# Kernel tuning notes

Hardware: AMD Instinct MI355X
Metric: run time of the kernel (lower is better)

## Reference

```python
import jax, jax.numpy as jnp
import numpy as np


def sage_conv(x, src, dst, n, W_l, b_l, W_r):
    # PyG SAGEConv (mean aggr): out = lin_l(mean_{j in N(i)} x_j) + lin_r(x_i)
    msg = x[src]                                            # [E, d_in] gather
    s = jax.ops.segment_sum(msg, dst, num_segments=n)       # [N, d_in]
    cnt = jax.ops.segment_sum(jnp.ones((src.shape[0], 1), x.dtype), dst, num_segments=n)
    mean = s / jnp.maximum(cnt, 1.0)
    return mean @ W_l.T + b_l + x @ W_r.T


def setup_inputs() -> dict:
    key = jax.random.key(0)
    ks = jax.random.split(key, 12)
    N, E, D = 200000, 6400000, 128
    x = jax.random.normal(ks[0], (N, D), dtype=jnp.float32)
    edge_index = jax.random.randint(ks[1], (2, E), 0, N, dtype=jnp.int64)

    def lin(k, dout, din, scale=None):
        s = scale if scale is not None else 1.0 / np.sqrt(din)
        return jax.random.uniform(k, (dout, din), jnp.float32, -s, s)

    return {
        "x": x,
        "edge_index": edge_index,
        "W1_l": lin(ks[2], 64, D), "b1_l": jnp.zeros((64,), jnp.float32), "W1_r": lin(ks[3], 64, D),
        "W2_l": lin(ks[4], 32, 64), "b2_l": jnp.zeros((32,), jnp.float32), "W2_r": lin(ks[5], 32, 64),
        "W3_l": lin(ks[6], 16, 32), "b3_l": jnp.zeros((16,), jnp.float32), "W3_r": lin(ks[7], 16, 32),
        "W_reg": lin(ks[8], 1, 16), "b_reg": jnp.zeros((1,), jnp.float32),
        "W_cls": lin(ks[9], 1, 16), "b_cls": jnp.zeros((1,), jnp.float32),
    }


def reference(x, edge_index, W1_l, b1_l, W1_r, W2_l, b2_l, W2_r, W3_l, b3_l, W3_r,
              W_reg, b_reg, W_cls, b_cls):
    # eval mode: dropout is identity
    n = x.shape[0]
    src, dst = edge_index[0], edge_index[1]
    h = jax.nn.relu(sage_conv(x, src, dst, n, W1_l, b1_l, W1_r))
    h = jax.nn.relu(sage_conv(h, src, dst, n, W2_l, b2_l, W2_r))
    h = jax.nn.relu(sage_conv(h, src, dst, n, W3_l, b3_l, W3_r))
    reg = (h @ W_reg.T + b_reg)[:, 0]
    cls = (h @ W_cls.T + b_cls)[:, 0]
    return (reg, cls)
```

## Files before the change

kernel.cpp:

```cpp
#include <hip/hip_runtime.h>


typedef __bf16 bf16x8 __attribute__((ext_vector_type(8)));
typedef float  f32x4  __attribute__((ext_vector_type(4)));
typedef int    i32x4  __attribute__((ext_vector_type(4)));

__device__ __forceinline__ unsigned short f2bf_rne(float f) {
    unsigned int u = __float_as_uint(f);
    u = (u + 0x7FFFu + ((u >> 16) & 1u)) >> 16;
    return (unsigned short)u;
}

__device__ __forceinline__ void bfacc(float4& a, const uint2 q) {
    a.x += __uint_as_float(q.x << 16);
    a.y += __uint_as_float(q.x & 0xFFFF0000u);
    a.z += __uint_as_float(q.y << 16);
    a.w += __uint_as_float(q.y & 0xFFFF0000u);
}


__global__ __launch_bounds__(256) void k_bcount(const int* __restrict__ dst, int E, int N,
                                                int* __restrict__ bcnt) {
    __shared__ int h[256];
    const int tid = threadIdx.x;
    h[tid] = 0;
    __syncthreads();
    const int stride = gridDim.x * 256;
    for (int i = blockIdx.x * 256 + tid; i < E; i += stride) {
        int d = dst[i];
        d = d < 0 ? 0 : (d >= N ? N - 1 : d);
        atomicAdd(&h[d >> 10], 1);
    }
    __syncthreads();
    if (h[tid]) atomicAdd(&bcnt[tid], h[tid]);
}

__global__ __launch_bounds__(256) void k_bscan(const int* __restrict__ bcnt,
                                               int* __restrict__ boff,
                                               int* __restrict__ bcur, int NBK, int E) {
    __shared__ int sd[256];
    const int tid = threadIdx.x;
    bcur[tid] = 0;
    int v = (tid < NBK) ? bcnt[tid] : 0;
    sd[tid] = v; __syncthreads();
    for (int off = 1; off < 256; off <<= 1) {
        int t = (tid >= off) ? sd[tid - off] : 0;
        __syncthreads();
        sd[tid] += t;
        __syncthreads();
    }
    if (tid < NBK) boff[tid] = sd[tid] - v;
    if (tid == 0) boff[NBK] = E;
}

#define BTILE 4096
__global__ __launch_bounds__(256) void k_bucket(const int* __restrict__ src,
                                                const int* __restrict__ dst, int E, int N,
                                                const int* __restrict__ boff,
                                                int* __restrict__ bcur,
                                                int* __restrict__ T, int NBK) {
    __shared__ int cnt[256], cnt2[256], lofs[256], gbase[256], boffs[256], sd[256];
    __shared__ int2 staged[BTILE];
    const int tid = threadIdx.x;
    const int tb = blockIdx.x * BTILE;
    const int tn = min(BTILE, E - tb);
    cnt[tid] = 0; cnt2[tid] = 0;
    boffs[tid] = (tid < NBK) ? boff[tid] : 0;
    __syncthreads();
    for (int i = tid; i < tn; i += 256) {
        int d = dst[tb + i];
        d = d < 0 ? 0 : (d >= N ? N - 1 : d);
        atomicAdd(&cnt[d >> 10], 1);
    }
    __syncthreads();
    int v = cnt[tid];
    sd[tid] = v; __syncthreads();
    for (int off = 1; off < 256; off <<= 1) {
        int t = (tid >= off) ? sd[tid - off] : 0;
        __syncthreads();
        sd[tid] += t;
        __syncthreads();
    }
    lofs[tid] = sd[tid] - v;
    if (v > 0 && tid < NBK) gbase[tid] = atomicAdd(&bcur[tid], v);
    __syncthreads();
    for (int i = tid; i < tn; i += 256) {
        int d = dst[tb + i];
        d = d < 0 ? 0 : (d >= N ? N - 1 : d);
        int s = src[tb + i];
        s = s < 0 ? 0 : (s >= N ? N - 1 : s);
        int b = d >> 10;
        int r = atomicAdd(&cnt2[b], 1);
        staged[lofs[b] + r] = make_int2(s, d);
    }
    __syncthreads();
    for (int i = tid; i < tn; i += 256) {
        int2 p = staged[i];
        int b = p.y >> 10;
        T[(size_t)boffs[b] + gbase[b] + (i - lofs[b])] = ((p.y & 1023) << 18) | p.x;
    }
}

__global__ __launch_bounds__(1024) void k_csr(const int* __restrict__ T,
                                              const int* __restrict__ boff,
                                              int* __restrict__ rowptr,
                                              int* __restrict__ adj, int N, int E) {
    __shared__ int hist[1024];
    __shared__ int sc[1024];
    const int tid = threadIdx.x;
    const int b = blockIdx.x;
    const int node0 = b << 10;
    hist[tid] = 0;
    __syncthreads();
    const int beg = boff[b], end = boff[b + 1];
    for (int i = beg + tid; i < end; i += 1024)
        atomicAdd(&hist[((unsigned)T[i]) >> 18], 1);
    __syncthreads();
    int v = hist[tid];
    sc[tid] = v;
    __syncthreads();
    for (int off = 1; off < 1024; off <<= 1) {
        int t = (tid >= off) ? sc[tid - off] : 0;
        __syncthreads();
        sc[tid] += t;
        __syncthreads();
    }
    const int excl = beg + sc[tid] - v;
    const int n = node0 + tid;
    if (n < N) rowptr[n] = excl;
    if (b == 0 && tid == 0) rowptr[N] = E;
    hist[tid] = excl;
    __syncthreads();
    for (int i = beg + tid; i < end; i += 1024) {
        unsigned p = (unsigned)T[i];
        int pos = atomicAdd(&hist[p >> 18], 1);
        adj[pos] = (int)(p & 0x3FFFFu);
    }
}

template<int DIN, int DOUT>
__global__ __launch_bounds__(256) void proj_mfma(const float* __restrict__ H,
                                                 const float* __restrict__ Wl,
                                                 const float* __restrict__ Wr,
                                                 const float* __restrict__ bias,
                                                 unsigned short* __restrict__ Pl,
                                                 float* __restrict__ R, int N) {
    constexpr int SP = DIN + 8;
    constexpr int COLT = DOUT / 16;
    __shared__ __bf16 lwl[DOUT * SP];
    __shared__ __bf16 lwrh[DOUT * SP];
    __shared__ __bf16 lwrl[DOUT * SP];
    for (int idx = threadIdx.x; idx < DIN * DOUT; idx += 256) {
        int c = idx / DIN, k = idx % DIN;
        float wl = Wl[idx], wr = Wr[idx];
        __bf16 wrh = (__bf16)wr;
        lwl[c * SP + k] = (__bf16)wl;
        lwrh[c * SP + k] = wrh;
        lwrl[c * SP + k] = (__bf16)(wr - (float)wrh);
    }
    __syncthreads();
    const int wave = threadIdx.x >> 6, lane = threadIdx.x & 63;
    const int quad = lane >> 4, l16 = lane & 15;
    const int n0 = (blockIdx.x * 4 + wave) * 16;
    int arow = n0 + l16;
    if (arow >= N) arow = N - 1;
    const float* hrow = H + (size_t)arow * DIN;

    f32x4 zero = {0.f, 0.f, 0.f, 0.f};
    f32x4 accP[COLT], accR[COLT];
    #pragma unroll
    for (int t = 0; t < COLT; ++t) { accP[t] = zero; accR[t] = zero; }

    for (int k0 = 0; k0 < DIN; k0 += 32) {
        const float* hp = hrow + k0 + quad * 8;
        float4 h0 = *(const float4*)hp;
        float4 h1 = *(const float4*)(hp + 4);
        float hv[8] = {h0.x, h0.y, h0.z, h0.w, h1.x, h1.y, h1.z, h1.w};
        bf16x8 ahi, alo;
        #pragma unroll
        for (int j = 0; j < 8; ++j) {
            __bf16 hb = (__bf16)hv[j];
            ahi[j] = hb;
            alo[j] = (__bf16)(hv[j] - (float)hb);
        }
        const int kk = k0 + quad * 8;
        #pragma unroll
        for (int t = 0; t < COLT; ++t) {
            const int c = t * 16 + l16;
            bf16x8 bl  = *(const bf16x8*)&lwl [c * SP + kk];
            bf16x8 brh = *(const bf16x8*)&lwrh[c * SP + kk];
            bf16x8 brl = *(const bf16x8*)&lwrl[c * SP + kk];
            accP[t] = __builtin_amdgcn_mfma_f32_16x16x32_bf16(ahi, bl,  accP[t], 0, 0, 0);
            accR[t] = __builtin_amdgcn_mfma_f32_16x16x32_bf16(ahi, brh, accR[t], 0, 0, 0);
            accR[t] = __builtin_amdgcn_mfma_f32_16x16x32_bf16(ahi, brl, accR[t], 0, 0, 0);
            accR[t] = __builtin_amdgcn_mfma_f32_16x16x32_bf16(alo, brh, accR[t], 0, 0, 0);
        }
    }
    #pragma unroll
    for (int t = 0; t < COLT; ++t) {
        const int c = t * 16 + l16;
        const float bc = bias[c];
        #pragma unroll
        for (int r = 0; r < 4; ++r) {
            int node = n0 + quad * 4 + r;
            if (node < N) {
                Pl[(size_t)node * DOUT + c] = f2bf_rne(accP[t][r]);
                R[(size_t)node * DOUT + c] = accR[t][r] + bc;
            }
        }
    }
}


template<int DOUT> struct GatherCfg {
    static constexpr int L   = DOUT / 4;
    static constexpr int S   = 64 / L;
    static constexpr int M   = 4;
    static constexpr int NPW = S * M;
    static constexpr int NPB = NPW * 4;
};

template<int DOUT, bool HEAD>
__global__ __launch_bounds__(256, 6) void gather_kernel(const unsigned short* __restrict__ P,
                                                        const int* __restrict__ rowptr,
                                                        const int* __restrict__ adj,
                                                        float* __restrict__ Hout, int N,
                                                        const float* __restrict__ Wreg,
                                                        const float* __restrict__ breg,
                                                        const float* __restrict__ Wcls,
                                                        const float* __restrict__ bcls,
                                                        float* __restrict__ out) {
    using C = GatherCfg<DOUT>;
    constexpr int L = C::L, S = C::S, M = C::M;
    constexpr int NPW = C::NPW, NPB = C::NPB;
    const int wave = threadIdx.x >> 6, lane = threadIdx.x & 63;
    const int sub = lane / L, cl = lane % L;
    const uint2* __restrict__ P2 = (const uint2*)P;
    f32x4* __restrict__ H4 = (f32x4*)Hout;
    const int base = blockIdx.x * NPB + wave * NPW + sub;
    #pragma unroll 1
    for (int m = 0; m < M; ++m) {
        int n = base + m * S;
        if (n >= N) continue;
        int beg = __builtin_nontemporal_load(rowptr + n);
        int end = __builtin_nontemporal_load(rowptr + n + 1);
        float4 a0 = {0, 0, 0, 0}, a1 = {0, 0, 0, 0}, a2 = {0, 0, 0, 0}, a3 = {0, 0, 0, 0};
        int j = beg;
        while (j < end && (j & 3)) { bfacc(a0, P2[(size_t)adj[j] * L + cl]); ++j; }
        for (; j + 8 <= end; j += 8) {
            i32x4 sA = __builtin_nontemporal_load((const i32x4*)(adj + j));
            i32x4 sB = __builtin_nontemporal_load((const i32x4*)(adj + j + 4));
            uint2 p0 = P2[(size_t)sA.x * L + cl];
            uint2 p1 = P2[(size_t)sA.y * L + cl];
            uint2 p2 = P2[(size_t)sA.z * L + cl];
            uint2 p3 = P2[(size_t)sA.w * L + cl];
            uint2 p4 = P2[(size_t)sB.x * L + cl];
            uint2 p5 = P2[(size_t)sB.y * L + cl];
            uint2 p6 = P2[(size_t)sB.z * L + cl];
            uint2 p7 = P2[(size_t)sB.w * L + cl];
            bfacc(a0, p0); bfacc(a1, p1); bfacc(a2, p2); bfacc(a3, p3);
            bfacc(a0, p4); bfacc(a1, p5); bfacc(a2, p6); bfacc(a3, p7);
        }
        if (j + 4 <= end) {
            i32x4 sA = __builtin_nontemporal_load((const i32x4*)(adj + j));
            bfacc(a0, P2[(size_t)sA.x * L + cl]);
            bfacc(a1, P2[(size_t)sA.y * L + cl]);
            bfacc(a2, P2[(size_t)sA.z * L + cl]);
            bfacc(a3, P2[(size_t)sA.w * L + cl]);
            j += 4;
        }
        for (; j < end; ++j) bfacc(a0, P2[(size_t)adj[j] * L + cl]);
        int deg = end - beg;
        float inv = deg > 0 ? 1.0f / (float)deg : 0.0f;
        f32x4 r = __builtin_nontemporal_load(&H4[(size_t)n * L + cl]);
        f32x4 o;
        o.x = fmaxf((a0.x + a1.x + a2.x + a3.x) * inv + r.x, 0.0f);
        o.y = fmaxf((a0.y + a1.y + a2.y + a3.y) * inv + r.y, 0.0f);
        o.z = fmaxf((a0.z + a1.z + a2.z + a3.z) * inv + r.z, 0.0f);
        o.w = fmaxf((a0.w + a1.w + a2.w + a3.w) * inv + r.w, 0.0f);
        if constexpr (HEAD) {
            float4 wr = ((const float4*)Wreg)[cl];
            float4 wc = ((const float4*)Wcls)[cl];
            float pr = o.x * wr.x + o.y * wr.y + o.z * wr.z + o.w * wr.w;
            float pc = o.x * wc.x + o.y * wc.y + o.z * wc.z + o.w * wc.w;
            pr += __shfl_xor(pr, 1); pr += __shfl_xor(pr, 2);
            pc += __shfl_xor(pc, 1); pc += __shfl_xor(pc, 2);
            if (cl == 0) {
                out[n] = pr + breg[0];
                out[(size_t)N + n] = pc + bcls[0];
            }
        } else {
            __builtin_nontemporal_store(o, &H4[(size_t)n * L + cl]);
        }
    }
}

extern "C" void kernel_launch(void* const* d_in, const int* in_sizes, int n_in,
                              void* d_out, int out_size, void* d_ws, size_t ws_size,
                              hipStream_t stream) {
    const float* x    = (const float*)d_in[0];
    const int*   ei   = (const int*)d_in[1];
    const float* W1l  = (const float*)d_in[2];
    const float* b1l  = (const float*)d_in[3];
    const float* W1r  = (const float*)d_in[4];
    const float* W2l  = (const float*)d_in[5];
    const float* b2l  = (const float*)d_in[6];
    const float* W2r  = (const float*)d_in[7];
    const float* W3l  = (const float*)d_in[8];
    const float* b3l  = (const float*)d_in[9];
    const float* W3r  = (const float*)d_in[10];
    const float* Wreg = (const float*)d_in[11];
    const float* breg = (const float*)d_in[12];
    const float* Wcls = (const float*)d_in[13];
    const float* bcls = (const float*)d_in[14];

    const int N = in_sizes[0] / 128;
    const int E = in_sizes[1] / 2;
    const int* src = ei;
    const int* dst = ei + E;

    char* ws = (char*)d_ws;
    size_t off = 0;
    auto alloc = [&](size_t bytes) -> void* {
        void* p = ws + off;
        off += (bytes + 255) & ~(size_t)255;
        return p;
    };
    int*   rowptr = (int*)alloc((size_t)(N + 1) * 4);
    int*   bcnt   = (int*)alloc(1024);
    int*   bcur   = (int*)alloc(1024);
    int*   boff   = (int*)alloc(1028);
    int*   adj    = (int*)alloc((size_t)E * 4);
    unsigned short* A = (unsigned short*)alloc((size_t)N * 64 * 2);
    float* B      = (float*)alloc((size_t)N * 64 * 4);
    float* C      = (float*)alloc((size_t)N * 32 * 4);
    float* D      = (float*)alloc((size_t)N * 16 * 4);
    int*   T      = (int*)B;

    const int NBK = (N + 1023) >> 10;

    hipMemsetAsync(bcnt, 0, 1024, stream);
    k_bcount<<<1024, 256, 0, stream>>>(dst, E, N, bcnt);
    k_bscan<<<1, 256, 0, stream>>>(bcnt, boff, bcur, NBK, E);
    k_bucket<<<(E + BTILE - 1) / BTILE, 256, 0, stream>>>(src, dst, E, N, boff, bcur, T, NBK);
    k_csr<<<NBK, 1024, 0, stream>>>(T, boff, rowptr, adj, N, E);

    const int PB = 64;
    constexpr int G64 = GatherCfg<64>::NPB;
    constexpr int G32 = GatherCfg<32>::NPB;
    constexpr int G16 = GatherCfg<16>::NPB;

    proj_mfma<128, 64><<<(N + PB - 1) / PB, 256, 0, stream>>>(x, W1l, W1r, b1l, A, B, N);
    gather_kernel<64, false><<<(N + G64 - 1) / G64, 256, 0, stream>>>(
        A, rowptr, adj, B, N, nullptr, nullptr, nullptr, nullptr, nullptr);
    proj_mfma<64, 32><<<(N + PB - 1) / PB, 256, 0, stream>>>(B, W2l, W2r, b2l, A, C, N);
    gather_kernel<32, false><<<(N + G32 - 1) / G32, 256, 0, stream>>>(
        A, rowptr, adj, C, N, nullptr, nullptr, nullptr, nullptr, nullptr);
    proj_mfma<32, 16><<<(N + PB - 1) / PB, 256, 0, stream>>>(C, W3l, W3r, b3l, A, D, N);
    gather_kernel<16, true><<<(N + G16 - 1) / G16, 256, 0, stream>>>(
        A, rowptr, adj, D, N, Wreg, breg, Wcls, bcls, (float*)d_out);
}
```

Measured before the change: 772.3 us.

## Fuse neighbor gather with next layer's projection via LDS staging

Merges each layer's mean-aggregation gather with the following layer's MFMA projection. The post-ReLU hidden rows are staged in shared memory and multiplied by the next weights, so the fp32 hidden activations are no longer written to and re-read from global memory. This also removes two kernel launches. It double-buffers the bf16 projection outputs (A1/A2) so a fused kernel never reads and writes the same buffer. It also drops the nontemporal load/store hints. In exchange there is more register and LDS pressure in the gather kernel, a block-wide barrier, and weights are reloaded and converted per block.

```diff
diff --git a/kernel.cpp b/kernel.cpp
--- a/kernel.cpp
+++ b/kernel.cpp
@@ -3,7 +3,6 @@
 
 typedef __bf16 bf16x8 __attribute__((ext_vector_type(8)));
 typedef float  f32x4  __attribute__((ext_vector_type(4)));
-typedef int    i32x4  __attribute__((ext_vector_type(4)));
 
 __device__ __forceinline__ unsigned short f2bf_rne(float f) {
     unsigned int u = __float_as_uint(f);
@@ -211,6 +210,137 @@
     }
 }
 
+template<int D, int DP>
+__global__ __launch_bounds__(256, 6) void gather_proj(const unsigned short* __restrict__ P,
+                                                      const int* __restrict__ rowptr,
+                                                      const int* __restrict__ adj,
+                                                      const float* __restrict__ Rres,
+                                                      const float* __restrict__ Wl,
+                                                      const float* __restrict__ Wr,
+                                                      const float* __restrict__ bias,
+                                                      unsigned short* __restrict__ Pout,
+                                                      float* __restrict__ Rout, int N) {
+    constexpr int L   = D / 4;
+    constexpr int S   = 64 / L;
+    constexpr int M   = 4;
+    constexpr int NPW = S * M;
+    constexpr int NPB = NPW * 4;
+    constexpr int SP  = D + 4;
+    constexpr int COLT = DP / 16;
+    __shared__ __align__(16) float hstage[NPB * SP];
+
+    const int wave = threadIdx.x >> 6, lane = threadIdx.x & 63;
+    const int sub = lane / L, cl = lane % L;
+    const uint2* __restrict__ P2 = (const uint2*)P;
+    const f32x4* __restrict__ R4 = (const f32x4*)Rres;
+    const int base = blockIdx.x * NPB + wave * NPW + sub;
+
+    #pragma unroll 1
+    for (int m = 0; m < M; ++m) {
+        const int n = base + m * S;
+        const int lrow = wave * NPW + sub + m * S;
+        f32x4 o = {0.f, 0.f, 0.f, 0.f};
+        if (n < N) {
+            int beg = rowptr[n], end = rowptr[n + 1];
+            float4 a0 = {0, 0, 0, 0}, a1 = {0, 0, 0, 0}, a2 = {0, 0, 0, 0}, a3 = {0, 0, 0, 0};
+            int j = beg;
+            while (j < end && (j & 3)) { bfacc(a0, P2[(size_t)adj[j] * L + cl]); ++j; }
+            for (; j + 8 <= end; j += 8) {
+                int4 sA = *(const int4*)(adj + j);
+                int4 sB = *(const int4*)(adj + j + 4);
+                uint2 p0 = P2[(size_t)sA.x * L + cl];
+                uint2 p1 = P2[(size_t)sA.y * L + cl];
+                uint2 p2 = P2[(size_t)sA.z * L + cl];
+                uint2 p3 = P2[(size_t)sA.w * L + cl];
+                uint2 p4 = P2[(size_t)sB.x * L + cl];
+                uint2 p5 = P2[(size_t)sB.y * L + cl];
+                uint2 p6 = P2[(size_t)sB.z * L + cl];
+                uint2 p7 = P2[(size_t)sB.w * L + cl];
+                bfacc(a0, p0); bfacc(a1, p1); bfacc(a2, p2); bfacc(a3, p3);
+                bfacc(a0, p4); bfacc(a1, p5); bfacc(a2, p6); bfacc(a3, p7);
+            }
+            if (j + 4 <= end) {
+                int4 sA = *(const int4*)(adj + j);
+                bfacc(a0, P2[(size_t)sA.x * L + cl]);
+                bfacc(a1, P2[(size_t)sA.y * L + cl]);
+                bfacc(a2, P2[(size_t)sA.z * L + cl]);
+                bfacc(a3, P2[(size_t)sA.w * L + cl]);
+                j += 4;
+            }
+            for (; j < end; ++j) bfacc(a0, P2[(size_t)adj[j] * L + cl]);
+            int deg = end - beg;
+            float inv = deg > 0 ? 1.0f / (float)deg : 0.0f;
+            f32x4 r = R4[(size_t)n * L + cl];
+            o.x = fmaxf((a0.x + a1.x + a2.x + a3.x) * inv + r.x, 0.0f);
+            o.y = fmaxf((a0.y + a1.y + a2.y + a3.y) * inv + r.y, 0.0f);
+            o.z = fmaxf((a0.z + a1.z + a2.z + a3.z) * inv + r.z, 0.0f);
+            o.w = fmaxf((a0.w + a1.w + a2.w + a3.w) * inv + r.w, 0.0f);
+        }
+        *(f32x4*)&hstage[lrow * SP + cl * 4] = o;
+    }
+    __syncthreads();
+
+    const int quad = lane >> 4, l16 = lane & 15;
+    f32x4 zero = {0.f, 0.f, 0.f, 0.f};
+    #pragma unroll
+    for (int tile = 0; tile < NPB / 64; ++tile) {
+        const int trow0 = wave * NPW + tile * 16;
+        f32x4 accP[COLT], accR[COLT];
+        #pragma unroll
+        for (int t = 0; t < COLT; ++t) { accP[t] = zero; accR[t] = zero; }
+        #pragma unroll
+        for (int k0 = 0; k0 < D; k0 += 32) {
+            const int kk = k0 + quad * 8;
+            const float* hp = &hstage[(trow0 + l16) * SP + kk];
+            bf16x8 ahi, alo;
+            #pragma unroll
+            for (int j = 0; j < 8; ++j) {
+                float hv = hp[j];
+                __bf16 hb = (__bf16)hv;
+                ahi[j] = hb;
+                alo[j] = (__bf16)(hv - (float)hb);
+            }
+            #pragma unroll
+            for (int t = 0; t < COLT; ++t) {
+                const int c = t * 16 + l16;
+                const float* wlp = Wl + c * D + kk;
+                const float* wrp = Wr + c * D + kk;
+                float4 wl0 = *(const float4*)wlp;
+                float4 wl1 = *(const float4*)(wlp + 4);
+                float4 wr0 = *(const float4*)wrp;
+                float4 wr1 = *(const float4*)(wrp + 4);
+                float wlv[8] = {wl0.x, wl0.y, wl0.z, wl0.w, wl1.x, wl1.y, wl1.z, wl1.w};
+                float wrv[8] = {wr0.x, wr0.y, wr0.z, wr0.w, wr1.x, wr1.y, wr1.z, wr1.w};
+                bf16x8 bl, brh, brl;
+                #pragma unroll
+                for (int j = 0; j < 8; ++j) {
+                    bl[j] = (__bf16)wlv[j];
+                    __bf16 wh = (__bf16)wrv[j];
+                    brh[j] = wh;
+                    brl[j] = (__bf16)(wrv[j] - (float)wh);
+                }
+                accP[t] = __builtin_amdgcn_mfma_f32_16x16x32_bf16(ahi, bl,  accP[t], 0, 0, 0);
+                accR[t] = __builtin_amdgcn_mfma_f32_16x16x32_bf16(ahi, brh, accR[t], 0, 0, 0);
+                accR[t] = __builtin_amdgcn_mfma_f32_16x16x32_bf16(ahi, brl, accR[t], 0, 0, 0);
+                accR[t] = __builtin_amdgcn_mfma_f32_16x16x32_bf16(alo, brh, accR[t], 0, 0, 0);
+            }
+        }
+        #pragma unroll
+        for (int t = 0; t < COLT; ++t) {
+            const int c = t * 16 + l16;
+            const float bc = bias[c];
+            #pragma unroll
+            for (int r = 0; r < 4; ++r) {
+                int node = blockIdx.x * NPB + trow0 + quad * 4 + r;
+                if (node < N) {
+                    Pout[(size_t)node * DP + c] = f2bf_rne(accP[t][r]);
+                    Rout[(size_t)node * DP + c] = accR[t][r] + bc;
+                }
+            }
+        }
+    }
+}
+
 
 template<int DOUT> struct GatherCfg {
     static constexpr int L   = DOUT / 4;
@@ -220,36 +350,35 @@
     static constexpr int NPB = NPW * 4;
 };
 
-template<int DOUT, bool HEAD>
-__global__ __launch_bounds__(256, 6) void gather_kernel(const unsigned short* __restrict__ P,
-                                                        const int* __restrict__ rowptr,
-                                                        const int* __restrict__ adj,
-                                                        float* __restrict__ Hout, int N,
-                                                        const float* __restrict__ Wreg,
-                                                        const float* __restrict__ breg,
-                                                        const float* __restrict__ Wcls,
-                                                        const float* __restrict__ bcls,
-                                                        float* __restrict__ out) {
+template<int DOUT>
+__global__ __launch_bounds__(256, 6) void gather_head(const unsigned short* __restrict__ P,
+                                                      const int* __restrict__ rowptr,
+                                                      const int* __restrict__ adj,
+                                                      const float* __restrict__ Rres, int N,
+                                                      const float* __restrict__ Wreg,
+                                                      const float* __restrict__ breg,
+                                                      const float* __restrict__ Wcls,
+                                                      const float* __restrict__ bcls,
+                                                      float* __restrict__ out) {
     using C = GatherCfg<DOUT>;
     constexpr int L = C::L, S = C::S, M = C::M;
     constexpr int NPW = C::NPW, NPB = C::NPB;
     const int wave = threadIdx.x >> 6, lane = threadIdx.x & 63;
     const int sub = lane / L, cl = lane % L;
     const uint2* __restrict__ P2 = (const uint2*)P;
-    f32x4* __restrict__ H4 = (f32x4*)Hout;
+    const float4* __restrict__ R4 = (const float4*)Rres;
     const int base = blockIdx.x * NPB + wave * NPW + sub;
     #pragma unroll 1
     for (int m = 0; m < M; ++m) {
         int n = base + m * S;
         if (n >= N) continue;
-        int beg = __builtin_nontemporal_load(rowptr + n);
-        int end = __builtin_nontemporal_load(rowptr + n + 1);
+        int beg = rowptr[n], end = rowptr[n + 1];
         float4 a0 = {0, 0, 0, 0}, a1 = {0, 0, 0, 0}, a2 = {0, 0, 0, 0}, a3 = {0, 0, 0, 0};
         int j = beg;
         while (j < end && (j & 3)) { bfacc(a0, P2[(size_t)adj[j] * L + cl]); ++j; }
         for (; j + 8 <= end; j += 8) {
-            i32x4 sA = __builtin_nontemporal_load((const i32x4*)(adj + j));
-            i32x4 sB = __builtin_nontemporal_load((const i32x4*)(adj + j + 4));
+            int4 sA = *(const int4*)(adj + j);
+            int4 sB = *(const int4*)(adj + j + 4);
             uint2 p0 = P2[(size_t)sA.x * L + cl];
             uint2 p1 = P2[(size_t)sA.y * L + cl];
             uint2 p2 = P2[(size_t)sA.z * L + cl];
@@ -262,7 +391,7 @@
             bfacc(a0, p4); bfacc(a1, p5); bfacc(a2, p6); bfacc(a3, p7);
         }
         if (j + 4 <= end) {
-            i32x4 sA = __builtin_nontemporal_load((const i32x4*)(adj + j));
+            int4 sA = *(const int4*)(adj + j);
             bfacc(a0, P2[(size_t)sA.x * L + cl]);
             bfacc(a1, P2[(size_t)sA.y * L + cl]);
             bfacc(a2, P2[(size_t)sA.z * L + cl]);
@@ -272,25 +401,21 @@
         for (; j < end; ++j) bfacc(a0, P2[(size_t)adj[j] * L + cl]);
         int deg = end - beg;
         float inv = deg > 0 ? 1.0f / (float)deg : 0.0f;
-        f32x4 r = __builtin_nontemporal_load(&H4[(size_t)n * L + cl]);
-        f32x4 o;
+        float4 r = R4[(size_t)n * L + cl];
+        float4 o;
         o.x = fmaxf((a0.x + a1.x + a2.x + a3.x) * inv + r.x, 0.0f);
         o.y = fmaxf((a0.y + a1.y + a2.y + a3.y) * inv + r.y, 0.0f);
         o.z = fmaxf((a0.z + a1.z + a2.z + a3.z) * inv + r.z, 0.0f);
         o.w = fmaxf((a0.w + a1.w + a2.w + a3.w) * inv + r.w, 0.0f);
-        if constexpr (HEAD) {
-            float4 wr = ((const float4*)Wreg)[cl];
-            float4 wc = ((const float4*)Wcls)[cl];
-            float pr = o.x * wr.x + o.y * wr.y + o.z * wr.z + o.w * wr.w;
-            float pc = o.x * wc.x + o.y * wc.y + o.z * wc.z + o.w * wc.w;
-            pr += __shfl_xor(pr, 1); pr += __shfl_xor(pr, 2);
-            pc += __shfl_xor(pc, 1); pc += __shfl_xor(pc, 2);
-            if (cl == 0) {
-                out[n] = pr + breg[0];
-                out[(size_t)N + n] = pc + bcls[0];
-            }
-        } else {
-            __builtin_nontemporal_store(o, &H4[(size_t)n * L + cl]);
+        float4 wr = ((const float4*)Wreg)[cl];
+        float4 wc = ((const float4*)Wcls)[cl];
+        float pr = o.x * wr.x + o.y * wr.y + o.z * wr.z + o.w * wr.w;
+        float pc = o.x * wc.x + o.y * wc.y + o.z * wc.z + o.w * wc.w;
+        pr += __shfl_xor(pr, 1); pr += __shfl_xor(pr, 2);
+        pc += __shfl_xor(pc, 1); pc += __shfl_xor(pc, 2);
+        if (cl == 0) {
+            out[n] = pr + breg[0];
+            out[(size_t)N + n] = pc + bcls[0];
         }
     }
 }
@@ -331,11 +456,13 @@
     int*   bcur   = (int*)alloc(1024);
     int*   boff   = (int*)alloc(1028);
     int*   adj    = (int*)alloc((size_t)E * 4);
-    unsigned short* A = (unsigned short*)alloc((size_t)N * 64 * 2);
+    unsigned short* A1 = (unsigned short*)alloc((size_t)N * 64 * 2);
+    unsigned short* A2 = (unsigned short*)alloc((size_t)N * 32 * 2);
     float* B      = (float*)alloc((size_t)N * 64 * 4);
     float* C      = (float*)alloc((size_t)N * 32 * 4);
     float* D      = (float*)alloc((size_t)N * 16 * 4);
     int*   T      = (int*)B;
+    unsigned short* A3 = A1;
 
     const int NBK = (N + 1023) >> 10;
 
@@ -346,17 +473,13 @@
     k_csr<<<NBK, 1024, 0, stream>>>(T, boff, rowptr, adj, N, E);
 
     const int PB = 64;
-    constexpr int G64 = GatherCfg<64>::NPB;
-    constexpr int G32 = GatherCfg<32>::NPB;
+
+    proj_mfma<128, 64><<<(N + PB - 1) / PB, 256, 0, stream>>>(x, W1l, W1r, b1l, A1, B, N);
+    gather_proj<64, 32><<<(N + 63) / 64, 256, 0, stream>>>(
+        A1, rowptr, adj, B, W2l, W2r, b2l, A2, C, N);
+    gather_proj<32, 16><<<(N + 127) / 128, 256, 0, stream>>>(
+        A2, rowptr, adj, C, W3l, W3r, b3l, A3, D, N);
     constexpr int G16 = GatherCfg<16>::NPB;
-
-    proj_mfma<128, 64><<<(N + PB - 1) / PB, 256, 0, stream>>>(x, W1l, W1r, b1l, A, B, N);
-    gather_kernel<64, false><<<(N + G64 - 1) / G64, 256, 0, stream>>>(
-        A, rowptr, adj, B, N, nullptr, nullptr, nullptr, nullptr, nullptr);
-    proj_mfma<64, 32><<<(N + PB - 1) / PB, 256, 0, stream>>>(B, W2l, W2r, b2l, A, C, N);
-    gather_kernel<32, false><<<(N + G32 - 1) / G32, 256, 0, stream>>>(
-        A, rowptr, adj, C, N, nullptr, nullptr, nullptr, nullptr, nullptr);
-    proj_mfma<32, 16><<<(N + PB - 1) / PB, 256, 0, stream>>>(C, W3l, W3r, b3l, A, D, N);
-    gather_kernel<16, true><<<(N + G16 - 1) / G16, 256, 0, stream>>>(
-        A, rowptr, adj, D, N, Wreg, breg, Wcls, bcls, (float*)d_out);
-}
+    gather_head<16><<<(N + G16 - 1) / G16, 256, 0, stream>>>(
+        A3, rowptr, adj, D, N, Wreg, breg, Wcls, bcls, (float*)d_out);
+}
```

After: 708.3 us. -8.3%, faster.
